# Optimization experiments

Measured on AMD Instinct MI355X. Metric: run time of the kernel, lower is better.

The kernel has to match this reference:

```python
import jax, jax.numpy as jnp
from jax import lax
import numpy as np

EPS = 1e-5
N_OBS_STEPS = 2

def _layernorm(x, g, b):
    m = jnp.mean(x, -1, keepdims=True)
    v = jnp.mean((x - m) ** 2, -1, keepdims=True)
    return (x - m) * lax.rsqrt(v + EPS) * g + b

def _fps(pc, num_points):
    # pc: [B, N, 3]; iterative farthest point sampling, start at index 0
    B, N, _ = pc.shape
    dist0 = jnp.full((B, N), jnp.inf, pc.dtype)
    far0 = jnp.zeros((B,), jnp.int32)
    def step(carry, _):
        dist, far = carry
        centroid = jnp.take_along_axis(pc, far[:, None, None], axis=1)  # [B,1,3]
        d = jnp.sum((pc - centroid) ** 2, -1)                            # [B,N]
        dist = jnp.minimum(dist, d)
        nxt = jnp.argmax(dist, -1).astype(jnp.int32)
        return (dist, nxt), far
    _, idx = lax.scan(step, (dist0, far0), None, length=num_points)
    idx = idx.T  # [B, num_points]
    return jnp.take_along_axis(pc, idx[..., None], axis=1)

def setup_inputs() -> dict:
    key = jax.random.key(0)
    ks = jax.random.split(key, 16)
    B, N, S = 256, 8192, 32
    def lin(k, i, o):
        return jax.random.normal(k, (i, o), jnp.float32) / np.sqrt(i)
    inp = {
        'point_cloud': jax.random.normal(ks[0], (B, N, 3), jnp.float32),
        'joint_state': jax.random.normal(ks[1], (B, S), jnp.float32),
        'num_points': 2048,
        'w1': lin(ks[2], 3, 64),   'b1': jnp.zeros((64,)),  'g1': jnp.ones((64,)),  'be1': jnp.zeros((64,)),
        'w2': lin(ks[3], 64, 128), 'b2': jnp.zeros((128,)), 'g2': jnp.ones((128,)), 'be2': jnp.zeros((128,)),
        'w3': lin(ks[4], 128, 256),'b3': jnp.zeros((256,)), 'g3': jnp.ones((256,)), 'be3': jnp.zeros((256,)),
        'wp': lin(ks[5], 256, 64), 'bp': jnp.zeros((64,)),  'gp': jnp.ones((64,)),  'bep': jnp.zeros((64,)),
        'ws1': lin(ks[6], S, 64),  'bs1': jnp.zeros((64,)),
        'ws2': lin(ks[7], 64, 64), 'bs2': jnp.zeros((64,)),
    }
    return inp

def reference(point_cloud, joint_state, num_points,
              w1, b1, g1, be1, w2, b2, g2, be2, w3, b3, g3, be3,
              wp, bp, gp, bep, ws1, bs1, ws2, bs2):
    pc = point_cloud[..., :3]
    pc = _fps(pc, num_points)                               # [B, num_points, 3]
    # PointNet pointwise MLP: 3->64->128->256 with LN+ReLU
    h = jax.nn.relu(_layernorm(pc @ w1 + b1, g1, be1))
    h = jax.nn.relu(_layernorm(h @ w2 + b2, g2, be2))
    h = jax.nn.relu(_layernorm(h @ w3 + b3, g3, be3))
    g = jnp.max(h, axis=1)                                  # global max pool [B,256]
    global_token = _layernorm(g @ wp + bp, gp, bep)         # [B,64]
    # State MLP: S->64->64 with ReLU between
    s = jax.nn.relu(joint_state @ ws1 + bs1)
    s = s @ ws2 + bs2                                       # [B,64]
    feat = jnp.concatenate([global_token, s], axis=-1)      # [B,128]
    B = feat.shape[0] // N_OBS_STEPS
    return feat.reshape(B, -1)                              # film conditioning
```

## Files before the change

### kernel.cpp

```cpp
#include <hip/hip_runtime.h>
#include <hip/hip_bf16.h>

#define EPS 1e-5f

typedef __attribute__((ext_vector_type(8))) short short8;
typedef __attribute__((ext_vector_type(4))) float floatx4;
typedef __attribute__((ext_vector_type(2))) float f32x2;

static __device__ __forceinline__ short f2bf(float f) {
    __hip_bfloat16 h = __float2bfloat16(f);
    return *reinterpret_cast<short*>(&h);
}

__global__ __launch_bounds__(256) void prep_kernel(const float* __restrict__ w2,
                                                   const float* __restrict__ w3,
                                                   short* __restrict__ w2T,
                                                   short* __restrict__ w3T,
                                                   int* __restrict__ gmax) {
    int i = blockIdx.x * 256 + threadIdx.x;
    if (i < 8192) {
        int k = i >> 7, n = i & 127;
        w2T[n * 64 + k] = f2bf(w2[i]);
    } else if (i < 40960) {
        int j = i - 8192;
        int k = j >> 8, n = j & 255;
        w3T[n * 128 + k] = f2bf(w3[j]);
    }
    if (i < 256 * 256) gmax[i] = 0;
}

#define DPP_MAXU64(pk, CTRL, RM)                                             \
    {                                                                        \
        int lo_ = (int)(unsigned)((pk) & 0xffffffffull);                     \
        int hi_ = (int)(unsigned)((pk) >> 32);                               \
        int nlo_ = __builtin_amdgcn_update_dpp(lo_, lo_, CTRL, RM, 0xf, false); \
        int nhi_ = __builtin_amdgcn_update_dpp(hi_, hi_, CTRL, RM, 0xf, false); \
        unsigned long long o_ =                                              \
            ((unsigned long long)(unsigned)nhi_ << 32) | (unsigned)nlo_;     \
        if (o_ > (pk)) (pk) = o_;                                            \
    }

__global__ __launch_bounds__(1024, 4) void fps_kernel(const float* __restrict__ pc,
                                                      float* __restrict__ sampled) {
#pragma clang fp contract(off)
    const int b = blockIdx.x;
    const int tid = threadIdx.x;
    const int lane = tid & 63;
    const float* __restrict__ P = pc + (size_t)b * 8192 * 3;
    float* __restrict__ outp = sampled + (size_t)b * 2048 * 3;

    __shared__ float sx[8192];
    __shared__ float sy[8192];
    __shared__ float sz[8192];
    __shared__ float sout[2048 * 3];
    __shared__ unsigned long long slots[3];

    f32x2 px2[4], py2[4], pz2[4], d2[4];
#pragma unroll
    for (int j = 0; j < 4; ++j) {
        int i0 = j * 2048 + tid;
        int i1 = j * 2048 + 1024 + tid;
        float x0 = P[i0 * 3 + 0], y0 = P[i0 * 3 + 1], z0 = P[i0 * 3 + 2];
        float x1 = P[i1 * 3 + 0], y1 = P[i1 * 3 + 1], z1 = P[i1 * 3 + 2];
        px2[j][0] = x0; px2[j][1] = x1;
        py2[j][0] = y0; py2[j][1] = y1;
        pz2[j][0] = z0; pz2[j][1] = z1;
        d2[j][0] = INFINITY; d2[j][1] = INFINITY;
        sx[i0] = x0; sy[i0] = y0; sz[i0] = z0;
        sx[i1] = x1; sy[i1] = y1; sz[i1] = z1;
    }
    if (tid < 3) slots[tid] = 0ull;
    __syncthreads();

    int far = 0;
    int p = 0;
    for (int s = 0; s < 2048; ++s) {
        const float cx = sx[far];
        const float cy = sy[far];
        const float cz = sz[far];
        if (tid == 0) {
            sout[s * 3 + 0] = cx;
            sout[s * 3 + 1] = cy;
            sout[s * 3 + 2] = cz;
        }
        if (s == 2047) break;

        const f32x2 c2x = {cx, cx}, c2y = {cy, cy}, c2z = {cz, cz};
        float bv_lo = -1.0f, bv_hi = -1.0f;
        int bj_lo = 0, bj_hi = 0;
#pragma unroll
        for (int j = 0; j < 4; ++j) {
            f32x2 dx = px2[j] - c2x;
            f32x2 dy = py2[j] - c2y;
            f32x2 dz = pz2[j] - c2z;
            f32x2 dd = (dx * dx + dy * dy) + dz * dz;
            f32x2 old = d2[j];
            f32x2 nd;
            nd[0] = fminf(old[0], dd[0]);
            nd[1] = fminf(old[1], dd[1]);
            d2[j] = nd;
            if (nd[0] > bv_lo) { bv_lo = nd[0]; bj_lo = j; }
            if (nd[1] > bv_hi) { bv_hi = nd[1]; bj_hi = j; }
        }
        float bv; int bi;
        if (bv_hi > bv_lo) { bv = bv_hi; bi = bj_hi * 2048 + 1024 + tid; }
        else               { bv = bv_lo; bi = bj_lo * 2048 + tid; }

        unsigned long long pk =
            ((unsigned long long)__float_as_uint(bv) << 32) | (unsigned)(8191 - bi);

        DPP_MAXU64(pk, 0x111, 0xf);
        DPP_MAXU64(pk, 0x112, 0xf);
        DPP_MAXU64(pk, 0x114, 0xf);
        DPP_MAXU64(pk, 0x118, 0xf);
        DPP_MAXU64(pk, 0x142, 0xa);
        DPP_MAXU64(pk, 0x143, 0xc);

        if (lane == 63)
            atomicMax(&slots[p], pk);
        __syncthreads();

        unsigned long long best = slots[p];
        if (tid == 0)
            slots[p >= 1 ? p - 1 : 2] = 0ull;
        far = 8191 - (int)(unsigned)(best & 0xFFFFFFFFull);
        p = (p == 2) ? 0 : p + 1;
    }

    __syncthreads();
#pragma unroll
    for (int i = 0; i < 6; ++i)
        outp[i * 1024 + tid] = sout[i * 1024 + tid];
}

__global__ __launch_bounds__(256) void mlp_kernel(
    const float* __restrict__ sampled,
    const float* __restrict__ w1, const float* __restrict__ b1,
    const float* __restrict__ g1, const float* __restrict__ be1,
    const short* __restrict__ w2T, const float* __restrict__ b2,
    const float* __restrict__ g2, const float* __restrict__ be2,
    const short* __restrict__ w3T, const float* __restrict__ b3,
    const float* __restrict__ g3, const float* __restrict__ be3,
    int* __restrict__ gmax) {

    const int b = blockIdx.x >> 5;
    const int chunk = blockIdx.x & 31;
    const int tid = threadIdx.x;
    const int w = tid >> 6;
    const int lane = tid & 63;
    const int quad = lane >> 4;
    const int col = lane & 15;

    __shared__ __align__(16) short X1[64 * 72];
    __shared__ __align__(16) char bufB[64 * 136 * 2];
    __shared__ float statsS[64 * 65];
    __shared__ float statsQ[64 * 65];
    __shared__ float mean_s[64];
    __shared__ float inv_s[64];

    float* Y1 = reinterpret_cast<float*>(bufB);
    short* X2 = reinterpret_cast<short*>(bufB);

    short8 b2f[2][2];
#pragma unroll
    for (int nt = 0; nt < 2; ++nt)
#pragma unroll
        for (int ks = 0; ks < 2; ++ks)
            b2f[nt][ks] = *(const short8*)&w2T[((w * 2 + nt) * 16 + col) * 64 + ks * 32 + quad * 8];
    short8 b3f[4][4];
#pragma unroll
    for (int nt = 0; nt < 4; ++nt)
#pragma unroll
        for (int ks = 0; ks < 4; ++ks)
            b3f[nt][ks] = *(const short8*)&w3T[((w * 4 + nt) * 16 + col) * 128 + ks * 32 + quad * 8];

    const int pt = tid & 63;
    const int cg = (tid >> 6) * 16;
    const float* Pp = &sampled[((size_t)b * 2048 + chunk * 64 + pt) * 3];
    const float x = Pp[0], y = Pp[1], z = Pp[2];
#pragma unroll
    for (int c = 0; c < 16; ++c) {
        int ch = cg + c;
        Y1[pt * 65 + ch] = fmaf(x, w1[ch], fmaf(y, w1[64 + ch], fmaf(z, w1[128 + ch], b1[ch])));
    }
    __syncthreads();

    if (tid < 64) {
        float s = 0.f, q = 0.f;
        for (int k = 0; k < 64; ++k) {
            float v = Y1[tid * 65 + k];
            s += v; q += v * v;
        }
        float m = s * (1.f / 64.f);
        float var = q * (1.f / 64.f) - m * m;
        mean_s[tid] = m;
        inv_s[tid] = rsqrtf(var + EPS);
    }
    __syncthreads();

#pragma unroll
    for (int c = 0; c < 16; ++c) {
        int ch = cg + c;
        float v = (Y1[pt * 65 + ch] - mean_s[pt]) * inv_s[pt] * g1[ch] + be1[ch];
        X1[pt * 72 + ch] = f2bf(fmaxf(v, 0.f));
    }
    __syncthreads();

    const floatx4 zf = {0.f, 0.f, 0.f, 0.f};
    floatx4 acc2[4][2];
#pragma unroll
    for (int mt = 0; mt < 4; ++mt) {
        acc2[mt][0] = zf; acc2[mt][1] = zf;
        short8 a[2];
#pragma unroll
        for (int ks = 0; ks < 2; ++ks)
            a[ks] = *(const short8*)&X1[(mt * 16 + col) * 72 + ks * 32 + quad * 8];
#pragma unroll
        for (int nt = 0; nt < 2; ++nt)
#pragma unroll
            for (int ks = 0; ks < 2; ++ks)
                acc2[mt][nt] = __builtin_amdgcn_mfma_f32_16x16x32_bf16(a[ks], b2f[nt][ks], acc2[mt][nt], 0, 0, 0);
    }
    int ch2[2];
    float b2v[2], g2v[2], be2v[2];
#pragma unroll
    for (int nt = 0; nt < 2; ++nt) {
        ch2[nt] = (w * 2 + nt) * 16 + col;
        b2v[nt] = b2[ch2[nt]]; g2v[nt] = g2[ch2[nt]]; be2v[nt] = be2[ch2[nt]];
    }
#pragma unroll
    for (int mt = 0; mt < 4; ++mt)
#pragma unroll
        for (int r = 0; r < 4; ++r) {
            float v0 = acc2[mt][0][r] + b2v[0];
            float v1 = acc2[mt][1][r] + b2v[1];
            acc2[mt][0][r] = v0; acc2[mt][1][r] = v1;
            int p = mt * 16 + quad * 4 + r;
            statsS[p * 65 + w * 16 + col] = v0 + v1;
            statsQ[p * 65 + w * 16 + col] = v0 * v0 + v1 * v1;
        }
    __syncthreads();
    if (tid < 64) {
        float s = 0.f, q = 0.f;
        for (int k = 0; k < 64; ++k) { s += statsS[tid * 65 + k]; q += statsQ[tid * 65 + k]; }
        float m = s * (1.f / 128.f);
        float var = q * (1.f / 128.f) - m * m;
        mean_s[tid] = m;
        inv_s[tid] = rsqrtf(var + EPS);
    }
    __syncthreads();
#pragma unroll
    for (int mt = 0; mt < 4; ++mt)
#pragma unroll
        for (int r = 0; r < 4; ++r) {
            int p = mt * 16 + quad * 4 + r;
            float m = mean_s[p], iv = inv_s[p];
#pragma unroll
            for (int nt = 0; nt < 2; ++nt) {
                float v = (acc2[mt][nt][r] - m) * iv * g2v[nt] + be2v[nt];
                X2[p * 136 + ch2[nt]] = f2bf(fmaxf(v, 0.f));
            }
        }
    __syncthreads();

    floatx4 acc3[4][4];
#pragma unroll
    for (int mt = 0; mt < 4; ++mt) {
#pragma unroll
        for (int nt = 0; nt < 4; ++nt) acc3[mt][nt] = zf;
        short8 a[4];
#pragma unroll
        for (int ks = 0; ks < 4; ++ks)
            a[ks] = *(const short8*)&X2[(mt * 16 + col) * 136 + ks * 32 + quad * 8];
#pragma unroll
        for (int nt = 0; nt < 4; ++nt)
#pragma unroll
            for (int ks = 0; ks < 4; ++ks)
                acc3[mt][nt] = __builtin_amdgcn_mfma_f32_16x16x32_bf16(a[ks], b3f[nt][ks], acc3[mt][nt], 0, 0, 0);
    }
    int ch3[4];
    float b3v[4], g3v[4], be3v[4];
#pragma unroll
    for (int nt = 0; nt < 4; ++nt) {
        ch3[nt] = (w * 4 + nt) * 16 + col;
        b3v[nt] = b3[ch3[nt]]; g3v[nt] = g3[ch3[nt]]; be3v[nt] = be3[ch3[nt]];
    }
#pragma unroll
    for (int mt = 0; mt < 4; ++mt)
#pragma unroll
        for (int r = 0; r < 4; ++r) {
            float s = 0.f, q = 0.f;
#pragma unroll
            for (int nt = 0; nt < 4; ++nt) {
                float v = acc3[mt][nt][r] + b3v[nt];
                acc3[mt][nt][r] = v;
                s += v; q += v * v;
            }
            int p = mt * 16 + quad * 4 + r;
            statsS[p * 65 + w * 16 + col] = s;
            statsQ[p * 65 + w * 16 + col] = q;
        }
    __syncthreads();
    if (tid < 64) {
        float s = 0.f, q = 0.f;
        for (int k = 0; k < 64; ++k) { s += statsS[tid * 65 + k]; q += statsQ[tid * 65 + k]; }
        float m = s * (1.f / 256.f);
        float var = q * (1.f / 256.f) - m * m;
        mean_s[tid] = m;
        inv_s[tid] = rsqrtf(var + EPS);
    }
    __syncthreads();

    float mx[4] = {0.f, 0.f, 0.f, 0.f};
#pragma unroll
    for (int mt = 0; mt < 4; ++mt)
#pragma unroll
        for (int r = 0; r < 4; ++r) {
            int p = mt * 16 + quad * 4 + r;
            float m = mean_s[p], iv = inv_s[p];
#pragma unroll
            for (int nt = 0; nt < 4; ++nt) {
                float v = (acc3[mt][nt][r] - m) * iv * g3v[nt] + be3v[nt];
                mx[nt] = fmaxf(mx[nt], fmaxf(v, 0.f));
            }
        }
#pragma unroll
    for (int nt = 0; nt < 4; ++nt) {
        float m = mx[nt];
        m = fmaxf(m, __shfl_xor(m, 16));
        m = fmaxf(m, __shfl_xor(m, 32));
        if (lane < 16)
            atomicMax(&gmax[b * 256 + ch3[nt]], __float_as_int(m));
    }
}

__global__ __launch_bounds__(64) void final_kernel(
    const float* __restrict__ g, const float* __restrict__ js,
    const float* __restrict__ wp, const float* __restrict__ bp,
    const float* __restrict__ gp, const float* __restrict__ bep,
    const float* __restrict__ ws1, const float* __restrict__ bs1,
    const float* __restrict__ ws2, const float* __restrict__ bs2,
    float* __restrict__ out) {
    const int b = blockIdx.x;
    const int c = threadIdx.x;

    const float* grow = g + b * 256;
    float acc = bp[c];
    for (int k = 0; k < 256; ++k) acc = fmaf(grow[k], wp[k * 64 + c], acc);
    float s = acc;
#pragma unroll
    for (int m = 1; m < 64; m <<= 1) s += __shfl_xor(s, m);
    float mean = s * (1.f / 64.f);
    float dc = acc - mean;
    float q = dc * dc;
#pragma unroll
    for (int m = 1; m < 64; m <<= 1) q += __shfl_xor(q, m);
    float var = q * (1.f / 64.f);
    out[b * 128 + c] = dc * rsqrtf(var + EPS) * gp[c] + bep[c];

    const float* jrow = js + b * 32;
    float h = bs1[c];
    for (int k = 0; k < 32; ++k) h = fmaf(jrow[k], ws1[k * 64 + c], h);
    h = fmaxf(h, 0.f);
    float s2 = bs2[c];
    for (int k = 0; k < 64; ++k) s2 = fmaf(__shfl(h, k), ws2[k * 64 + c], s2);
    out[b * 128 + 64 + c] = s2;
}

extern "C" void kernel_launch(void* const* d_in, const int* in_sizes, int n_in,
                              void* d_out, int out_size, void* d_ws, size_t ws_size,
                              hipStream_t stream) {
    const float* pc  = (const float*)d_in[0];
    const float* js  = (const float*)d_in[1];
    const float* w1  = (const float*)d_in[3];
    const float* b1  = (const float*)d_in[4];
    const float* g1  = (const float*)d_in[5];
    const float* be1 = (const float*)d_in[6];
    const float* w2  = (const float*)d_in[7];
    const float* b2  = (const float*)d_in[8];
    const float* g2  = (const float*)d_in[9];
    const float* be2 = (const float*)d_in[10];
    const float* w3  = (const float*)d_in[11];
    const float* b3  = (const float*)d_in[12];
    const float* g3  = (const float*)d_in[13];
    const float* be3 = (const float*)d_in[14];
    const float* wp  = (const float*)d_in[15];
    const float* bp  = (const float*)d_in[16];
    const float* gp  = (const float*)d_in[17];
    const float* bep = (const float*)d_in[18];
    const float* ws1 = (const float*)d_in[19];
    const float* bs1 = (const float*)d_in[20];
    const float* ws2 = (const float*)d_in[21];
    const float* bs2 = (const float*)d_in[22];

    char* ws = (char*)d_ws;
    float* sampled = (float*)(ws + 0);
    int*   gmax    = (int*)(ws + 6291456);
    short* w2T     = (short*)(ws + 6553600);
    short* w3T     = (short*)(ws + 6569984);

    prep_kernel<<<256, 256, 0, stream>>>(w2, w3, w2T, w3T, gmax);
    fps_kernel<<<256, 1024, 0, stream>>>(pc, sampled);
    mlp_kernel<<<8192, 256, 0, stream>>>(sampled, w1, b1, g1, be1,
                                         w2T, b2, g2, be2, w3T, b3, g3, be3, gmax);
    final_kernel<<<256, 64, 0, stream>>>((const float*)gmax, js, wp, bp, gp, bep,
                                         ws1, bs1, ws2, bs2, (float*)d_out);
}
```

Measured before the change: 2.550 ms.

## Shrink FPS blocks to 256 threads with 32 points per thread in registers

The FPS kernel moves from 1024 threads holding 8 points each (packed float2 math) to 256 threads holding 32 points each in scalar registers. The per-step distance update and running argmax are rewritten as a scalar loop using fmaxf and a select. Four wavefronts instead of sixteen should make the per-step atomic max and __syncthreads barrier cheaper, since FPS runs 2048 dependent steps. In exchange each thread does four times the arithmetic per step, there are fewer wavefronts to hide latency, and register pressure rises while the packed-FP32 vectorization is given up.

```diff
diff --git a/kernel.cpp b/kernel.cpp
--- a/kernel.cpp
+++ b/kernel.cpp
@@ -5,7 +5,6 @@
 
 typedef __attribute__((ext_vector_type(8))) short short8;
 typedef __attribute__((ext_vector_type(4))) float floatx4;
-typedef __attribute__((ext_vector_type(2))) float f32x2;
 
 static __device__ __forceinline__ short f2bf(float f) {
     __hip_bfloat16 h = __float2bfloat16(f);
@@ -40,8 +39,8 @@
         if (o_ > (pk)) (pk) = o_;                                            \
     }
 
-__global__ __launch_bounds__(1024, 4) void fps_kernel(const float* __restrict__ pc,
-                                                      float* __restrict__ sampled) {
+__global__ __launch_bounds__(256, 1) void fps_kernel(const float* __restrict__ pc,
+                                                     float* __restrict__ sampled) {
 #pragma clang fp contract(off)
     const int b = blockIdx.x;
     const int tid = threadIdx.x;
@@ -55,19 +54,14 @@
     __shared__ float sout[2048 * 3];
     __shared__ unsigned long long slots[3];
 
-    f32x2 px2[4], py2[4], pz2[4], d2[4];
-#pragma unroll
-    for (int j = 0; j < 4; ++j) {
-        int i0 = j * 2048 + tid;
-        int i1 = j * 2048 + 1024 + tid;
+    float px[32], py[32], pz[32], d[32];
+#pragma unroll
+    for (int j = 0; j < 32; ++j) {
+        int i0 = j * 256 + tid;
         float x0 = P[i0 * 3 + 0], y0 = P[i0 * 3 + 1], z0 = P[i0 * 3 + 2];
-        float x1 = P[i1 * 3 + 0], y1 = P[i1 * 3 + 1], z1 = P[i1 * 3 + 2];
-        px2[j][0] = x0; px2[j][1] = x1;
-        py2[j][0] = y0; py2[j][1] = y1;
-        pz2[j][0] = z0; pz2[j][1] = z1;
-        d2[j][0] = INFINITY; d2[j][1] = INFINITY;
+        px[j] = x0; py[j] = y0; pz[j] = z0;
+        d[j] = INFINITY;
         sx[i0] = x0; sy[i0] = y0; sz[i0] = z0;
-        sx[i1] = x1; sy[i1] = y1; sz[i1] = z1;
     }
     if (tid < 3) slots[tid] = 0ull;
     __syncthreads();
@@ -85,26 +79,20 @@
         }
         if (s == 2047) break;
 
-        const f32x2 c2x = {cx, cx}, c2y = {cy, cy}, c2z = {cz, cz};
-        float bv_lo = -1.0f, bv_hi = -1.0f;
-        int bj_lo = 0, bj_hi = 0;
-#pragma unroll
-        for (int j = 0; j < 4; ++j) {
-            f32x2 dx = px2[j] - c2x;
-            f32x2 dy = py2[j] - c2y;
-            f32x2 dz = pz2[j] - c2z;
-            f32x2 dd = (dx * dx + dy * dy) + dz * dz;
-            f32x2 old = d2[j];
-            f32x2 nd;
-            nd[0] = fminf(old[0], dd[0]);
-            nd[1] = fminf(old[1], dd[1]);
-            d2[j] = nd;
-            if (nd[0] > bv_lo) { bv_lo = nd[0]; bj_lo = j; }
-            if (nd[1] > bv_hi) { bv_hi = nd[1]; bj_hi = j; }
-        }
-        float bv; int bi;
-        if (bv_hi > bv_lo) { bv = bv_hi; bi = bj_hi * 2048 + 1024 + tid; }
-        else               { bv = bv_lo; bi = bj_lo * 2048 + tid; }
+        float bv = -1.0f;
+        int bj = 0;
+#pragma unroll
+        for (int j = 0; j < 32; ++j) {
+            float dx = px[j] - cx;
+            float dy = py[j] - cy;
+            float dz = pz[j] - cz;
+            float dd = (dx * dx + dy * dy) + dz * dz;
+            float nd = fminf(d[j], dd);
+            d[j] = nd;
+            bj = (nd > bv) ? j : bj;
+            bv = fmaxf(bv, nd);
+        }
+        int bi = (bj << 8) + tid;
 
         unsigned long long pk =
             ((unsigned long long)__float_as_uint(bv) << 32) | (unsigned)(8191 - bi);
@@ -129,8 +117,8 @@
 
     __syncthreads();
 #pragma unroll
-    for (int i = 0; i < 6; ++i)
-        outp[i * 1024 + tid] = sout[i * 1024 + tid];
+    for (int i = 0; i < 24; ++i)
+        outp[i * 256 + tid] = sout[i * 256 + tid];
 }
 
 __global__ __launch_bounds__(256) void mlp_kernel(
@@ -400,7 +388,7 @@
     short* w3T     = (short*)(ws + 6569984);
 
     prep_kernel<<<256, 256, 0, stream>>>(w2, w3, w2T, w3T, gmax);
-    fps_kernel<<<256, 1024, 0, stream>>>(pc, sampled);
+    fps_kernel<<<256, 256, 0, stream>>>(pc, sampled);
     mlp_kernel<<<8192, 256, 0, stream>>>(sampled, w1, b1, g1, be1,
                                          w2T, b2, g2, be2, w3T, b3, g3, be3, gmax);
     final_kernel<<<256, 64, 0, stream>>>((const float*)gmax, js, wp, bp, gp, bep,
```

New measurement: 2.290 ms. 10.2% less time.
